# Performance work log

Measured on AMD Instinct MI355X. Metric: run time of the kernel, lower is better.

The kernel has to match this reference:

```python
import jax, jax.numpy as jnp
import numpy as np

N_NODES = 50000
N_EDGES = 1280000
N_GRAPHS = 64
IN_CH = 6
HID = 64
SLOPE = 0.2  # LeakyReLU negative slope


def _lrelu(x):
    return jax.nn.leaky_relu(x, SLOPE)


def _edge_conv(x, src, dst, W1, b1, W2, b2):
    # PyG EdgeConv: message = nn([x_i, x_j - x_i]); x_i = x[dst], x_j = x[src]; max-aggr onto dst
    xi = x[dst]                                   # [E, F]
    m = jnp.concatenate([xi, x[src] - xi], -1)    # [E, 2F]
    h = _lrelu(_lrelu(m @ W1 + b1) @ W2 + b2)     # [E, H]
    agg = jax.ops.segment_max(h, dst, num_segments=N_NODES)
    return jnp.where(jnp.isneginf(agg), 0.0, agg)  # nodes with no in-edges -> 0


def setup_inputs() -> dict:
    key = jax.random.key(0)
    ks = jax.random.split(key, 12)
    glorot = lambda k, fi, fo: jax.random.normal(k, (fi, fo), jnp.float32) * np.sqrt(2.0 / (fi + fo))
    x = jax.random.normal(ks[0], (N_NODES, IN_CH), jnp.float32)
    edge_index = jax.random.randint(ks[1], (2, N_EDGES), 0, N_NODES, jnp.int64 if jax.config.x64_enabled else jnp.int32)
    batch = jnp.sort(jax.random.randint(ks[2], (N_NODES,), 0, N_GRAPHS))
    return {
        "x": x, "edge_index": edge_index, "batch": batch,
        "W1": glorot(ks[3], 2 * IN_CH, HID), "b1": jnp.zeros((HID,), jnp.float32),
        "W2": glorot(ks[4], HID, HID),       "b2": jnp.zeros((HID,), jnp.float32),
        "W3": glorot(ks[5], 2 * HID, HID),   "b3": jnp.zeros((HID,), jnp.float32),
        "W4": glorot(ks[6], HID, HID),       "b4": jnp.zeros((HID,), jnp.float32),
        "Wc1": glorot(ks[7], 2 * HID, HID),  "bc1": jnp.zeros((HID,), jnp.float32),
        "Wc2": glorot(ks[8], HID, 1),        "bc2": jnp.zeros((1,), jnp.float32),
    }


def reference(x, edge_index, batch, W1, b1, W2, b2, W3, b3, W4, b4, Wc1, bc1, Wc2, bc2):
    src, dst = edge_index[0], edge_index[1]
    h = _edge_conv(x, src, dst, W1, b1, W2, b2)   # [N, H]
    h = _edge_conv(h, src, dst, W3, b3, W4, b4)   # [N, H]
    # global mean + max pool per graph
    cnt = jax.ops.segment_sum(jnp.ones((N_NODES,), h.dtype), batch, num_segments=N_GRAPHS)
    mean_p = jax.ops.segment_sum(h, batch, num_segments=N_GRAPHS) / jnp.clip(cnt, 1.0)[:, None]
    max_p = jax.ops.segment_max(h, batch, num_segments=N_GRAPHS)
    max_p = jnp.where(jnp.isneginf(max_p), 0.0, max_p)
    g = jnp.concatenate([mean_p, max_p], -1)      # [G, 2H]
    logits = _lrelu(g @ Wc1 + bc1) @ Wc2 + bc2    # dropout is identity at inference
    return logits.squeeze(-1)                      # [G]
```

## Files before the change

kernel.cpp:

```cpp
#include <hip/hip_runtime.h>
#include <hip/hip_bf16.h>

#define SLOPE 0.2f
#define NPB 64
#define CAP 2048
#define MAXBUCK 1024
#define EPB 4096
#define XF1B 512
#define PPARTS 16

typedef _Float16 f16x8  __attribute__((ext_vector_type(8)));
typedef float    f32x4  __attribute__((ext_vector_type(4)));
typedef unsigned u32;
typedef unsigned u32x4  __attribute__((ext_vector_type(4)));

__device__ __forceinline__ float lrelu(float v) { return fmaxf(v, SLOPE * v); }

__device__ __forceinline__ float lane_bcast(float v, int k) {
    return __int_as_float(__builtin_amdgcn_readlane(__float_as_int(v), k));
}

__device__ __forceinline__ f16x8 lrelu8(f16x8 v) {
    f16x8 s = v * (_Float16)SLOPE;
#if __has_builtin(__builtin_elementwise_max)
    return __builtin_elementwise_max(v, s);
#else
    f16x8 r;
#pragma unroll
    for (int i = 0; i < 8; ++i) r[i] = v[i] > s[i] ? v[i] : s[i];
    return r;
#endif
}

__device__ __forceinline__ void split_f16(float v, _Float16& h, _Float16& l) {
    h = (_Float16)v;
    l = (_Float16)(v - (float)h);
}
__device__ __forceinline__ u32 pack_f16(_Float16 a, _Float16 b) {
    return (u32)__builtin_bit_cast(unsigned short, a) |
           ((u32)__builtin_bit_cast(unsigned short, b) << 16);
}

__global__ void __launch_bounds__(256) scatter_xform1_kernel(
    const int* __restrict__ srcI, const int* __restrict__ dstI,
    int* __restrict__ cursor, u32* __restrict__ pairW,
    int E, int nNodes, int nBuck, int nCntB,
    const float* __restrict__ x,
    const float* __restrict__ W1, const float* __restrict__ b1,
    _Float16* __restrict__ Ph, _Float16* __restrict__ Qh)
{
    if (blockIdx.x < nCntB) {
        __shared__ int cnt[MAXBUCK];
        __shared__ int base[MAXBUCK];
        const int tid = threadIdx.x;
        const int e0 = blockIdx.x * EPB;
        const int e1 = min(e0 + EPB, E);

        for (int b = tid; b < nBuck; b += 256) cnt[b] = 0;
        __syncthreads();
        for (int e = e0 + tid; e < e1; e += 256)
            atomicAdd(&cnt[dstI[e] >> 6], 1);
        __syncthreads();
        for (int b = tid; b < nBuck; b += 256) {
            int c = cnt[b];
            base[b] = (c > 0) ? (b * CAP + atomicAdd(&cursor[b], c)) : 0;
            cnt[b] = 0;
        }
        __syncthreads();
        for (int e = e0 + tid; e < e1; e += 256) {
            const int d = dstI[e];
            const int b = d >> 6;
            const int loc = atomicAdd(&cnt[b], 1);
            const int pos = min(base[b] + loc, b * CAP + CAP - 1);
            pairW[pos] = ((u32)srcI[e] << 6) | (u32)(d & (NPB - 1));
        }
        return;
    }
    const int lane = threadIdx.x & 63;
    const int wave = ((blockIdx.x - nCntB) * 256 + threadIdx.x) >> 6;
    const int nw   = (XF1B * 256) >> 6;

    float wd[6], wb[6];
#pragma unroll
    for (int r = 0; r < 6; ++r) {
        wb[r] = W1[(6 + r) * 64 + lane];
        wd[r] = W1[r * 64 + lane] - wb[r];
    }
    const float bb = b1[lane];
    for (int i = wave; i < nNodes; i += nw) {
        const float* xr = x + (size_t)i * 6;
        float p = bb, q = 0.f;
#pragma unroll
        for (int r = 0; r < 6; ++r) {
            float xv = xr[r];
            p = fmaf(xv, wd[r], p);
            q = fmaf(xv, wb[r], q);
        }
        Ph[(size_t)i * 64 + lane] = (_Float16)p;
        Qh[(size_t)i * 64 + lane] = (_Float16)q;
    }
}

__global__ void __launch_bounds__(256) bucket_sort_kernel(
    const u32* __restrict__ pairW, const int* __restrict__ cursor,
    int2* __restrict__ rowInfo, int* __restrict__ sortedSrc, int nNodes)
{
    __shared__ int nodeCnt[NPB];
    __shared__ int nodeCur[NPB];
    const int b   = blockIdx.x;
    const int n0  = b * NPB;
    const int n1  = min(n0 + NPB, nNodes);
    const int tid = threadIdx.x;
    if (tid < NPB) nodeCnt[tid] = 0;
    __syncthreads();
    const int r0 = b * CAP;
    const int r1 = r0 + min(cursor[b], CAP);
    for (int i = r0 + tid; i < r1; i += 256)
        atomicAdd(&nodeCnt[pairW[i] & (NPB - 1)], 1);
    __syncthreads();
    if (tid < 64) {
        const int c = nodeCnt[tid];
        int inc = c;
#pragma unroll
        for (int off = 1; off < 64; off <<= 1) {
            int t = __shfl_up(inc, off);
            if (tid >= off) inc += t;
        }
        const int st = r0 + inc - c;
        nodeCur[tid] = st;
        if (tid < n1 - n0) rowInfo[n0 + tid] = make_int2(st, c);
    }
    __syncthreads();
    for (int i = r0 + tid; i < r1; i += 256) {
        const u32 w = pairW[i];
        const int pos = atomicAdd(&nodeCur[w & (NPB - 1)], 1);
        sortedSrc[pos] = (int)(w >> 6);
    }
}

__global__ void __launch_bounds__(256) node_xform2_kernel(
    const float* __restrict__ A,
    const float* __restrict__ W3, const float* __restrict__ b3,
    _Float16* __restrict__ Ph, _Float16* __restrict__ Qh, int nNodes)
{
    const int lane = threadIdx.x & 63;
    const int wave = (blockIdx.x * blockDim.x + threadIdx.x) >> 6;
    const int nw   = (gridDim.x * blockDim.x) >> 6;

    float wd[64], wb[64];
#pragma unroll
    for (int k = 0; k < 64; ++k) {
        wb[k] = W3[(64 + k) * 64 + lane];
        wd[k] = W3[k * 64 + lane] - wb[k];
    }
    const float bb = b3[lane];

    for (int i = wave; i < nNodes; i += nw) {
        const float a = A[(size_t)i * 64 + lane];
        float p0 = bb, p1 = 0.f, p2 = 0.f, p3 = 0.f;
        float q0 = 0.f, q1 = 0.f, q2 = 0.f, q3 = 0.f;
#pragma unroll
        for (int k = 0; k < 64; k += 4) {
            float a0 = lane_bcast(a, k);
            float a1 = lane_bcast(a, k + 1);
            float a2 = lane_bcast(a, k + 2);
            float a3 = lane_bcast(a, k + 3);
            p0 = fmaf(a0, wd[k],     p0);  q0 = fmaf(a0, wb[k],     q0);
            p1 = fmaf(a1, wd[k + 1], p1);  q1 = fmaf(a1, wb[k + 1], q1);
            p2 = fmaf(a2, wd[k + 2], p2);  q2 = fmaf(a2, wb[k + 2], q2);
            p3 = fmaf(a3, wd[k + 3], p3);  q3 = fmaf(a3, wb[k + 3], q3);
        }
        Ph[(size_t)i * 64 + lane] = (_Float16)((p0 + p1) + (p2 + p3));
        Qh[(size_t)i * 64 + lane] = (_Float16)((q0 + q1) + (q2 + q3));
    }
}

__global__ void __launch_bounds__(256) edge_agg_mfma_kernel(
    const _Float16* __restrict__ Ph, const _Float16* __restrict__ Qh,
    const int2* __restrict__ rowInfo, const int* __restrict__ sortedSrc,
    const float* __restrict__ W, const float* __restrict__ b,
    float* __restrict__ outB, int nNodes)
{
    __shared__ u32x4 wlds[16][64];

    const int tid  = threadIdx.x;
    const int lane = tid & 63;
    const int cn   = lane & 15;
    const int q    = lane >> 4;
    const int wv   = tid >> 6;
    const int wave = (blockIdx.x * 256 + tid) >> 6;
    const int nw   = (gridDim.x * 256) >> 6;

#pragma unroll
    for (int i = 0; i < 4; ++i) {
        const int f    = wv + i * 4;
        const int isLo = f >> 3;
        const int g    = f & 7;
        const int nt   = g >> 1;
        const int ks   = g & 1;
        u32x4 d;
#pragma unroll
        for (int p = 0; p < 4; ++p) {
            float w0 = W[(ks * 32 + q * 8 + 2 * p)     * 64 + nt * 16 + cn];
            float w1 = W[(ks * 32 + q * 8 + 2 * p + 1) * 64 + nt * 16 + cn];
            _Float16 h0, l0, h1, l1;
            split_f16(w0, h0, l0);
            split_f16(w1, h1, l1);
            d[p] = isLo ? pack_f16(l0, l1) : pack_f16(h0, h1);
        }
        wlds[f][lane] = d;
    }
    float bc[4];
#pragma unroll
    for (int nt = 0; nt < 4; ++nt) bc[nt] = b[nt * 16 + cn];
    __syncthreads();

    const u32 nClamp = (u32)(nNodes - 1);

    for (int base = wave; base < nNodes; base += 2 * nw) {
        const int n1 = base;
        const int n2 = base + nw;
        const bool has2 = (n2 < nNodes);

        const int2 ri1 = rowInfo[n1];
        const int2 ri2 = has2 ? rowInfo[n2] : make_int2(ri1.x, 0);
        const int rs1  = __builtin_amdgcn_readfirstlane(ri1.x);
        const int deg1 = __builtin_amdgcn_readfirstlane(ri1.y);
        const int rs2  = __builtin_amdgcn_readfirstlane(ri2.x);
        const int deg2 = __builtin_amdgcn_readfirstlane(ri2.y);
        const int d1c = max(deg1, 1) - 1;
        const int d2c = max(deg2, 1) - 1;

        const f16x8* P1 = (const f16x8*)(Ph + (size_t)n1 * 64);
        const f16x8* P2 = (const f16x8*)(Ph + (size_t)(has2 ? n2 : n1) * 64);
        const f16x8 p1A = P1[q], p1B = P1[4 + q];
        const f16x8 p2A = P2[q], p2B = P2[4 + q];

        float m10 = -INFINITY, m11 = -INFINITY, m12 = -INFINITY, m13 = -INFINITY;
        float m20 = -INFINITY, m21 = -INFINITY, m22 = -INFINITY, m23 = -INFINITY;

        const int gmax = max(deg1, deg2);
        for (int g0 = 0; g0 < gmax; g0 += 32) {
            u32 sA1 = (u32)sortedSrc[rs1 + min(g0 + cn,      d1c)];
            u32 sB1 = (u32)sortedSrc[rs1 + min(g0 + 16 + cn, d1c)];
            u32 sA2 = (u32)sortedSrc[rs2 + min(g0 + cn,      d2c)];
            u32 sB2 = (u32)sortedSrc[rs2 + min(g0 + 16 + cn, d2c)];
            sA1 = min(sA1, nClamp); sB1 = min(sB1, nClamp);
            sA2 = min(sA2, nClamp); sB2 = min(sB2, nClamp);
            const f16x8* QA1 = (const f16x8*)(Qh + (size_t)sA1 * 64);
            const f16x8* QB1 = (const f16x8*)(Qh + (size_t)sB1 * 64);
            const f16x8* QA2 = (const f16x8*)(Qh + (size_t)sA2 * 64);
            const f16x8* QB2 = (const f16x8*)(Qh + (size_t)sB2 * 64);
            const f16x8 qA1a = QA1[q], qA1b = QA1[4 + q];
            const f16x8 qB1a = QB1[q], qB1b = QB1[4 + q];
            const f16x8 qA2a = QA2[q], qA2b = QA2[4 + q];
            const f16x8 qB2a = QB2[q], qB2b = QB2[4 + q];

            if (g0 < deg1) {
                const f16x8 A00 = lrelu8(p1A + qA1a);
                const f16x8 A01 = lrelu8(p1B + qA1b);
                const f16x8 A10 = lrelu8(p1A + qB1a);
                const f16x8 A11 = lrelu8(p1B + qB1b);
#pragma unroll
                for (int nt = 0; nt < 4; ++nt) {
                    const f16x8 wh0 = __builtin_bit_cast(f16x8, wlds[nt * 2][lane]);
                    const f16x8 wh1 = __builtin_bit_cast(f16x8, wlds[nt * 2 + 1][lane]);
                    const f16x8 wl0 = __builtin_bit_cast(f16x8, wlds[8 + nt * 2][lane]);
                    const f16x8 wl1 = __builtin_bit_cast(f16x8, wlds[8 + nt * 2 + 1][lane]);
                    f32x4 a; a[0] = a[1] = a[2] = a[3] = bc[nt];
                    a = __builtin_amdgcn_mfma_f32_16x16x32_f16(A00, wl0, a, 0, 0, 0);
                    a = __builtin_amdgcn_mfma_f32_16x16x32_f16(A00, wh0, a, 0, 0, 0);
                    a = __builtin_amdgcn_mfma_f32_16x16x32_f16(A01, wl1, a, 0, 0, 0);
                    a = __builtin_amdgcn_mfma_f32_16x16x32_f16(A01, wh1, a, 0, 0, 0);
                    f32x4 c; c[0] = c[1] = c[2] = c[3] = bc[nt];
                    c = __builtin_amdgcn_mfma_f32_16x16x32_f16(A10, wl0, c, 0, 0, 0);
                    c = __builtin_amdgcn_mfma_f32_16x16x32_f16(A10, wh0, c, 0, 0, 0);
                    c = __builtin_amdgcn_mfma_f32_16x16x32_f16(A11, wl1, c, 0, 0, 0);
                    c = __builtin_amdgcn_mfma_f32_16x16x32_f16(A11, wh1, c, 0, 0, 0);
                    float m = (nt == 0) ? m10 : (nt == 1) ? m11 : (nt == 2) ? m12 : m13;
                    m = fmaxf(m, fmaxf(fmaxf(a[0], a[1]), fmaxf(a[2], a[3])));
                    m = fmaxf(m, fmaxf(fmaxf(c[0], c[1]), fmaxf(c[2], c[3])));
                    if (nt == 0) m10 = m; else if (nt == 1) m11 = m;
                    else if (nt == 2) m12 = m; else m13 = m;
                }
            }
            if (g0 < deg2) {
                const f16x8 A00 = lrelu8(p2A + qA2a);
                const f16x8 A01 = lrelu8(p2B + qA2b);
                const f16x8 A10 = lrelu8(p2A + qB2a);
                const f16x8 A11 = lrelu8(p2B + qB2b);
#pragma unroll
                for (int nt = 0; nt < 4; ++nt) {
                    const f16x8 wh0 = __builtin_bit_cast(f16x8, wlds[nt * 2][lane]);
                    const f16x8 wh1 = __builtin_bit_cast(f16x8, wlds[nt * 2 + 1][lane]);
                    const f16x8 wl0 = __builtin_bit_cast(f16x8, wlds[8 + nt * 2][lane]);
                    const f16x8 wl1 = __builtin_bit_cast(f16x8, wlds[8 + nt * 2 + 1][lane]);
                    f32x4 a; a[0] = a[1] = a[2] = a[3] = bc[nt];
                    a = __builtin_amdgcn_mfma_f32_16x16x32_f16(A00, wl0, a, 0, 0, 0);
                    a = __builtin_amdgcn_mfma_f32_16x16x32_f16(A00, wh0, a, 0, 0, 0);
                    a = __builtin_amdgcn_mfma_f32_16x16x32_f16(A01, wl1, a, 0, 0, 0);
                    a = __builtin_amdgcn_mfma_f32_16x16x32_f16(A01, wh1, a, 0, 0, 0);
                    f32x4 c; c[0] = c[1] = c[2] = c[3] = bc[nt];
                    c = __builtin_amdgcn_mfma_f32_16x16x32_f16(A10, wl0, c, 0, 0, 0);
                    c = __builtin_amdgcn_mfma_f32_16x16x32_f16(A10, wh0, c, 0, 0, 0);
                    c = __builtin_amdgcn_mfma_f32_16x16x32_f16(A11, wl1, c, 0, 0, 0);
                    c = __builtin_amdgcn_mfma_f32_16x16x32_f16(A11, wh1, c, 0, 0, 0);
                    float m = (nt == 0) ? m20 : (nt == 1) ? m21 : (nt == 2) ? m22 : m23;
                    m = fmaxf(m, fmaxf(fmaxf(a[0], a[1]), fmaxf(a[2], a[3])));
                    m = fmaxf(m, fmaxf(fmaxf(c[0], c[1]), fmaxf(c[2], c[3])));
                    if (nt == 0) m20 = m; else if (nt == 1) m21 = m;
                    else if (nt == 2) m22 = m; else m23 = m;
                }
            }
        }

        m10 = fmaxf(m10, __shfl_xor(m10, 16)); m10 = fmaxf(m10, __shfl_xor(m10, 32));
        m11 = fmaxf(m11, __shfl_xor(m11, 16)); m11 = fmaxf(m11, __shfl_xor(m11, 32));
        m12 = fmaxf(m12, __shfl_xor(m12, 16)); m12 = fmaxf(m12, __shfl_xor(m12, 32));
        m13 = fmaxf(m13, __shfl_xor(m13, 16)); m13 = fmaxf(m13, __shfl_xor(m13, 32));
        float sel1 = (q < 2) ? ((q == 0) ? m10 : m11) : ((q == 2) ? m12 : m13);
        outB[(size_t)n1 * 64 + q * 16 + cn] = (deg1 > 0) ? lrelu(sel1) : 0.0f;

        if (has2) {
            m20 = fmaxf(m20, __shfl_xor(m20, 16)); m20 = fmaxf(m20, __shfl_xor(m20, 32));
            m21 = fmaxf(m21, __shfl_xor(m21, 16)); m21 = fmaxf(m21, __shfl_xor(m21, 32));
            m22 = fmaxf(m22, __shfl_xor(m22, 16)); m22 = fmaxf(m22, __shfl_xor(m22, 32));
            m23 = fmaxf(m23, __shfl_xor(m23, 16)); m23 = fmaxf(m23, __shfl_xor(m23, 32));
            float sel2 = (q < 2) ? ((q == 0) ? m20 : m21) : ((q == 2) ? m22 : m23);
            outB[(size_t)n2 * 64 + q * 16 + cn] = (deg2 > 0) ? lrelu(sel2) : 0.0f;
        }
    }
}

__device__ __forceinline__ int lower_bound_i(const int* __restrict__ a, int n, int key)
{
    int lo = 0, hi = n;
    while (lo < hi) {
        int mid = (lo + hi) >> 1;
        if (a[mid] < key) lo = mid + 1; else hi = mid;
    }
    return lo;
}

__global__ void __launch_bounds__(256) pool_kernel(
    const float* __restrict__ B, const int* __restrict__ batch,
    float* __restrict__ gpart, int nNodes)
{
    const int gid  = blockIdx.x / PPARTS;
    const int part = blockIdx.x % PPARTS;
    const int c    = threadIdx.x & 63;
    const int wid  = threadIdx.x >> 6;

    const int s = lower_bound_i(batch, nNodes, gid);
    const int e = lower_bound_i(batch, nNodes, gid + 1);
    const int len = e - s;
    const int ps = s + (len * part) / PPARTS;
    const int pe = s + (len * (part + 1)) / PPARTS;

    float sum = 0.f, mx = -INFINITY;
    for (int n = ps + wid; n < pe; n += 4) {
        float v = B[(size_t)n * 64 + c];
        sum += v;
        mx = fmaxf(mx, v);
    }
    __shared__ float ssum[4][64];
    __shared__ float smax[4][64];
    ssum[wid][c] = sum;
    smax[wid][c] = mx;
    __syncthreads();
    if (wid == 0) {
        sum = (ssum[0][c] + ssum[1][c]) + (ssum[2][c] + ssum[3][c]);
        mx  = fmaxf(fmaxf(smax[0][c], smax[1][c]), fmaxf(smax[2][c], smax[3][c]));
        float* row = gpart + (size_t)blockIdx.x * 132;
        row[c]      = sum;
        row[64 + c] = mx;
        if (c == 0) row[128] = (float)(pe - ps);
    }
}

__global__ void __launch_bounds__(64) cls_kernel(
    const float* __restrict__ gpart,
    const float* __restrict__ Wc1, const float* __restrict__ bc1,
    const float* __restrict__ Wc2, const float* __restrict__ bc2,
    float* __restrict__ out)
{
    __shared__ float g[128];
    const int gid = blockIdx.x;
    const int c   = threadIdx.x;

    float s = 0.f, m = -INFINITY, cnt = 0.f;
#pragma unroll
    for (int p = 0; p < PPARTS; ++p) {
        const float* row = gpart + (size_t)(gid * PPARTS + p) * 132;
        s += row[c];
        m = fmaxf(m, row[64 + c]);
        cnt += row[128];
    }
    g[c]      = s / fmaxf(cnt, 1.0f);
    g[64 + c] = (cnt > 0.f) ? m : 0.0f;
    __syncthreads();

    float t = bc1[c];
#pragma unroll 8
    for (int k = 0; k < 128; ++k) t = fmaf(g[k], Wc1[k * 64 + c], t);
    t = lrelu(t);
    float p = t * Wc2[c];
#pragma unroll
    for (int off = 32; off > 0; off >>= 1) p += __shfl_down(p, off);
    if (c == 0) out[gid] = p + bc2[0];
}

static inline size_t align_up(size_t v, size_t a) { return (v + a - 1) & ~(a - 1); }

extern "C" void kernel_launch(void* const* d_in, const int* in_sizes, int n_in,
                              void* d_out, int out_size, void* d_ws, size_t ws_size,
                              hipStream_t stream)
{
    const float* x     = (const float*)d_in[0];
    const int*   ei    = (const int*)d_in[1];
    const int*   batch = (const int*)d_in[2];
    const float* W1  = (const float*)d_in[3];
    const float* b1  = (const float*)d_in[4];
    const float* W2  = (const float*)d_in[5];
    const float* b2  = (const float*)d_in[6];
    const float* W3  = (const float*)d_in[7];
    const float* b3  = (const float*)d_in[8];
    const float* W4  = (const float*)d_in[9];
    const float* b4  = (const float*)d_in[10];
    const float* Wc1 = (const float*)d_in[11];
    const float* bc1 = (const float*)d_in[12];
    const float* Wc2 = (const float*)d_in[13];
    const float* bc2 = (const float*)d_in[14];
    float* out = (float*)d_out;

    const int nNodes  = in_sizes[0] / 6;
    const int E       = in_sizes[1] / 2;
    const int nGraphs = out_size;
    const int* srcI = ei;
    const int* dstI = ei + E;
    const int nBuck = (nNodes + NPB - 1) / NPB;
    const int nCntB = (E + EPB - 1) / EPB;

    char* wsp = (char*)d_ws;
    size_t off = 0;
    int*  cursor    = (int*)(wsp + off);   off = align_up(off + (size_t)MAXBUCK * 4, 256);
    int2* rowInfo   = (int2*)(wsp + off);  off = align_up(off + (size_t)nNodes * 8, 256);
    int*  sortedSrc = (int*)(wsp + off);   off = align_up(off + (size_t)nBuck * CAP * 4, 256);
    u32*  pairW     = (u32*)(wsp + off);   off = align_up(off + (size_t)nBuck * CAP * 4, 256);
    const size_t nFeat = (size_t)nNodes * 64;
    _Float16* Ph   = (_Float16*)(wsp + off);  off = align_up(off + nFeat * 2, 256);
    _Float16* Qh   = (_Float16*)(wsp + off);  off = align_up(off + nFeat * 2, 256);
    float*    B1   = (float*)(wsp + off);     off = align_up(off + nFeat * 4, 256);
    float*    B2   = (float*)(wsp + off);     off = align_up(off + nFeat * 4, 256);
    float*    gpart= (float*)(wsp + off);     off = align_up(off + (size_t)nGraphs * PPARTS * 132 * 4, 256);
    (void)ws_size;

    (void)hipMemsetAsync(cursor, 0, (size_t)nBuck * 4, stream);
    scatter_xform1_kernel<<<nCntB + XF1B, 256, 0, stream>>>(
        srcI, dstI, cursor, pairW, E, nNodes, nBuck, nCntB, x, W1, b1, Ph, Qh);
    bucket_sort_kernel<<<nBuck, 256, 0, stream>>>(pairW, cursor, rowInfo,
                                                  sortedSrc, nNodes);

    edge_agg_mfma_kernel<<<2048, 256, 0, stream>>>(Ph, Qh, rowInfo, sortedSrc,
                                                   W2, b2, B1, nNodes);
    node_xform2_kernel<<<2048, 256, 0, stream>>>(B1, W3, b3, Ph, Qh, nNodes);
    edge_agg_mfma_kernel<<<2048, 256, 0, stream>>>(Ph, Qh, rowInfo, sortedSrc,
                                                   W4, b4, B2, nNodes);

    pool_kernel<<<nGraphs * PPARTS, 256, 0, stream>>>(B2, batch, gpart, nNodes);
    cls_kernel<<<nGraphs, 64, 0, stream>>>(gpart, Wc1, bc1, Wc2, bc2, out);
}
```

Measured before the change: 274.2 us.

## Split bucket cursors into 8 sub-buckets and store node features in fp16

```diff
diff --git a/kernel.cpp b/kernel.cpp
--- a/kernel.cpp
+++ b/kernel.cpp
@@ -4,6 +4,7 @@
 #define SLOPE 0.2f
 #define NPB 64
 #define CAP 2048
+#define SUBCAP 384
 #define MAXBUCK 1024
 #define EPB 4096
 #define XF1B 512
@@ -53,6 +54,7 @@
         __shared__ int cnt[MAXBUCK];
         __shared__ int base[MAXBUCK];
         const int tid = threadIdx.x;
+        const int j   = blockIdx.x & 7;
         const int e0 = blockIdx.x * EPB;
         const int e1 = min(e0 + EPB, E);
 
@@ -63,7 +65,9 @@
         __syncthreads();
         for (int b = tid; b < nBuck; b += 256) {
             int c = cnt[b];
-            base[b] = (c > 0) ? (b * CAP + atomicAdd(&cursor[b], c)) : 0;
+            base[b] = (c > 0)
+                ? ((b * 8 + j) * SUBCAP + min(atomicAdd(&cursor[b * 8 + j], c), SUBCAP))
+                : 0;
             cnt[b] = 0;
         }
         __syncthreads();
@@ -71,7 +75,7 @@
             const int d = dstI[e];
             const int b = d >> 6;
             const int loc = atomicAdd(&cnt[b], 1);
-            const int pos = min(base[b] + loc, b * CAP + CAP - 1);
+            const int pos = min(base[b] + loc, (b * 8 + j + 1) * SUBCAP - 1);
             pairW[pos] = ((u32)srcI[e] << 6) | (u32)(d & (NPB - 1));
         }
         return;
@@ -113,10 +117,13 @@
     const int tid = threadIdx.x;
     if (tid < NPB) nodeCnt[tid] = 0;
     __syncthreads();
-    const int r0 = b * CAP;
-    const int r1 = r0 + min(cursor[b], CAP);
-    for (int i = r0 + tid; i < r1; i += 256)
-        atomicAdd(&nodeCnt[pairW[i] & (NPB - 1)], 1);
+#pragma unroll
+    for (int jj = 0; jj < 8; ++jj) {
+        const int w0 = (b * 8 + jj) * SUBCAP;
+        const int wc = min(cursor[b * 8 + jj], SUBCAP);
+        for (int i = w0 + tid; i < w0 + wc; i += 256)
+            atomicAdd(&nodeCnt[pairW[i] & (NPB - 1)], 1);
+    }
     __syncthreads();
     if (tid < 64) {
         const int c = nodeCnt[tid];
@@ -126,20 +133,25 @@
             int t = __shfl_up(inc, off);
             if (tid >= off) inc += t;
         }
-        const int st = r0 + inc - c;
+        const int st = b * CAP + inc - c;
         nodeCur[tid] = st;
         if (tid < n1 - n0) rowInfo[n0 + tid] = make_int2(st, c);
     }
     __syncthreads();
-    for (int i = r0 + tid; i < r1; i += 256) {
-        const u32 w = pairW[i];
-        const int pos = atomicAdd(&nodeCur[w & (NPB - 1)], 1);
-        sortedSrc[pos] = (int)(w >> 6);
+#pragma unroll
+    for (int jj = 0; jj < 8; ++jj) {
+        const int w0 = (b * 8 + jj) * SUBCAP;
+        const int wc = min(cursor[b * 8 + jj], SUBCAP);
+        for (int i = w0 + tid; i < w0 + wc; i += 256) {
+            const u32 w = pairW[i];
+            const int pos = atomicAdd(&nodeCur[w & (NPB - 1)], 1);
+            sortedSrc[pos] = (int)(w >> 6);
+        }
     }
 }
 
 __global__ void __launch_bounds__(256) node_xform2_kernel(
-    const float* __restrict__ A,
+    const _Float16* __restrict__ B1h,
     const float* __restrict__ W3, const float* __restrict__ b3,
     _Float16* __restrict__ Ph, _Float16* __restrict__ Qh, int nNodes)
 {
@@ -156,7 +168,7 @@
     const float bb = b3[lane];
 
     for (int i = wave; i < nNodes; i += nw) {
-        const float a = A[(size_t)i * 64 + lane];
+        const float a = (float)B1h[(size_t)i * 64 + lane];
         float p0 = bb, p1 = 0.f, p2 = 0.f, p3 = 0.f;
         float q0 = 0.f, q1 = 0.f, q2 = 0.f, q3 = 0.f;
 #pragma unroll
@@ -179,7 +191,7 @@
     const _Float16* __restrict__ Ph, const _Float16* __restrict__ Qh,
     const int2* __restrict__ rowInfo, const int* __restrict__ sortedSrc,
     const float* __restrict__ W, const float* __restrict__ b,
-    float* __restrict__ outB, int nNodes)
+    _Float16* __restrict__ outB, int nNodes)
 {
     __shared__ u32x4 wlds[16][64];
 
@@ -319,7 +331,8 @@
         m12 = fmaxf(m12, __shfl_xor(m12, 16)); m12 = fmaxf(m12, __shfl_xor(m12, 32));
         m13 = fmaxf(m13, __shfl_xor(m13, 16)); m13 = fmaxf(m13, __shfl_xor(m13, 32));
         float sel1 = (q < 2) ? ((q == 0) ? m10 : m11) : ((q == 2) ? m12 : m13);
-        outB[(size_t)n1 * 64 + q * 16 + cn] = (deg1 > 0) ? lrelu(sel1) : 0.0f;
+        outB[(size_t)n1 * 64 + q * 16 + cn] =
+            (_Float16)((deg1 > 0) ? lrelu(sel1) : 0.0f);
 
         if (has2) {
             m20 = fmaxf(m20, __shfl_xor(m20, 16)); m20 = fmaxf(m20, __shfl_xor(m20, 32));
@@ -327,7 +340,8 @@
             m22 = fmaxf(m22, __shfl_xor(m22, 16)); m22 = fmaxf(m22, __shfl_xor(m22, 32));
             m23 = fmaxf(m23, __shfl_xor(m23, 16)); m23 = fmaxf(m23, __shfl_xor(m23, 32));
             float sel2 = (q < 2) ? ((q == 0) ? m20 : m21) : ((q == 2) ? m22 : m23);
-            outB[(size_t)n2 * 64 + q * 16 + cn] = (deg2 > 0) ? lrelu(sel2) : 0.0f;
+            outB[(size_t)n2 * 64 + q * 16 + cn] =
+                (_Float16)((deg2 > 0) ? lrelu(sel2) : 0.0f);
         }
     }
 }
@@ -343,7 +357,7 @@
 }
 
 __global__ void __launch_bounds__(256) pool_kernel(
-    const float* __restrict__ B, const int* __restrict__ batch,
+    const _Float16* __restrict__ Bh, const int* __restrict__ batch,
     float* __restrict__ gpart, int nNodes)
 {
     const int gid  = blockIdx.x / PPARTS;
@@ -359,7 +373,7 @@
 
     float sum = 0.f, mx = -INFINITY;
     for (int n = ps + wid; n < pe; n += 4) {
-        float v = B[(size_t)n * 64 + c];
+        float v = (float)Bh[(size_t)n * 64 + c];
         sum += v;
         mx = fmaxf(mx, v);
     }
@@ -443,30 +457,30 @@
 
     char* wsp = (char*)d_ws;
     size_t off = 0;
-    int*  cursor    = (int*)(wsp + off);   off = align_up(off + (size_t)MAXBUCK * 4, 256);
+    int*  cursor    = (int*)(wsp + off);   off = align_up(off + (size_t)MAXBUCK * 8 * 4, 256);
     int2* rowInfo   = (int2*)(wsp + off);  off = align_up(off + (size_t)nNodes * 8, 256);
     int*  sortedSrc = (int*)(wsp + off);   off = align_up(off + (size_t)nBuck * CAP * 4, 256);
-    u32*  pairW     = (u32*)(wsp + off);   off = align_up(off + (size_t)nBuck * CAP * 4, 256);
+    u32*  pairW     = (u32*)(wsp + off);   off = align_up(off + (size_t)nBuck * 8 * SUBCAP * 4, 256);
     const size_t nFeat = (size_t)nNodes * 64;
     _Float16* Ph   = (_Float16*)(wsp + off);  off = align_up(off + nFeat * 2, 256);
     _Float16* Qh   = (_Float16*)(wsp + off);  off = align_up(off + nFeat * 2, 256);
-    float*    B1   = (float*)(wsp + off);     off = align_up(off + nFeat * 4, 256);
-    float*    B2   = (float*)(wsp + off);     off = align_up(off + nFeat * 4, 256);
+    _Float16* B1h  = (_Float16*)(wsp + off);  off = align_up(off + nFeat * 2, 256);
+    _Float16* B2h  = (_Float16*)(wsp + off);  off = align_up(off + nFeat * 2, 256);
     float*    gpart= (float*)(wsp + off);     off = align_up(off + (size_t)nGraphs * PPARTS * 132 * 4, 256);
     (void)ws_size;
 
-    (void)hipMemsetAsync(cursor, 0, (size_t)nBuck * 4, stream);
+    (void)hipMemsetAsync(cursor, 0, (size_t)nBuck * 8 * 4, stream);
     scatter_xform1_kernel<<<nCntB + XF1B, 256, 0, stream>>>(
         srcI, dstI, cursor, pairW, E, nNodes, nBuck, nCntB, x, W1, b1, Ph, Qh);
     bucket_sort_kernel<<<nBuck, 256, 0, stream>>>(pairW, cursor, rowInfo,
                                                   sortedSrc, nNodes);
 
     edge_agg_mfma_kernel<<<2048, 256, 0, stream>>>(Ph, Qh, rowInfo, sortedSrc,
-                                                   W2, b2, B1, nNodes);
-    node_xform2_kernel<<<2048, 256, 0, stream>>>(B1, W3, b3, Ph, Qh, nNodes);
+                                                   W2, b2, B1h, nNodes);
+    node_xform2_kernel<<<2048, 256, 0, stream>>>(B1h, W3, b3, Ph, Qh, nNodes);
     edge_agg_mfma_kernel<<<2048, 256, 0, stream>>>(Ph, Qh, rowInfo, sortedSrc,
-                                                   W4, b4, B2, nNodes);
-
-    pool_kernel<<<nGraphs * PPARTS, 256, 0, stream>>>(B2, batch, gpart, nNodes);
+                                                   W4, b4, B2h, nNodes);
+
+    pool_kernel<<<nGraphs * PPARTS, 256, 0, stream>>>(B2h, batch, gpart, nNodes);
     cls_kernel<<<nGraphs, 64, 0, stream>>>(gpart, Wc1, bc1, Wc2, bc2, out);
 }
```

Measured after the change: 272.5 us. No clear change (-0.6%).
